# Kernel optimization log

Measured on AMD Instinct MI355X. Metric: run time of the kernel, lower is better.

Reference implementation:

```python
import jax, jax.numpy as jnp
import numpy as np

DIM = 1024
HEADS = 8
NUM_EXPERTS = 65536
NUM_KEYS = 256  # sqrt(NUM_EXPERTS)
DIM_KEY = 512
TOPK = 16  # product_key_topk == num_experts_per_head


def setup_inputs() -> dict:
    key = jax.random.key(0)
    ks = jax.random.split(key, 6)
    B, N = 2, 512
    x = jax.random.normal(ks[0], (B, N, DIM), dtype=jnp.float32)
    gamma = jnp.ones((DIM,), dtype=jnp.float32)
    wq = jax.random.normal(ks[1], (2 * HEADS * DIM_KEY, DIM), dtype=jnp.float32) * 0.02
    keys = jax.random.normal(ks[2], (HEADS, NUM_KEYS, 2, DIM_KEY), dtype=jnp.float32) * 0.02
    table_down = jax.random.normal(ks[3], (NUM_EXPERTS, DIM), dtype=jnp.float32) * 0.02
    table_up = jax.random.normal(ks[4], (NUM_EXPERTS, DIM), dtype=jnp.float32) * 0.02
    return {"x": x, "gamma": gamma, "wq": wq, "keys": keys,
            "table_down": table_down, "table_up": table_up}


def _rmsnorm(v, g):
    # torch F.normalize(x, dim=-1) * gamma * sqrt(dim)
    scale = jnp.sqrt(jnp.asarray(v.shape[-1], v.dtype))
    n = jnp.maximum(jnp.linalg.norm(v, axis=-1, keepdims=True), 1e-12)
    return v / n * g * scale


def reference(x, gamma, wq, keys, table_down, table_up):
    B, N, D = x.shape
    xn = _rmsnorm(x, gamma)          # pre_rmsnorm on x
    gate = xn                        # x_in_gate is None -> gate = norm(x)
    # queries: b n (p h d) -> p b n h d
    q = gate @ wq.T                  # [B,N,2*H*DK]
    q = q.reshape(B, N, 2, HEADS, DIM_KEY).transpose(2, 0, 1, 3, 4)  # [2,B,N,H,DK]
    # sim: p b n h d, h k p d -> p b n h k
    sim = jnp.einsum('pbnhd,hkpd->pbnhk', q, keys)
    sx, ix = jax.lax.top_k(sim[0], TOPK)  # [B,N,H,TOPK]
    sy, iy = jax.lax.top_k(sim[1], TOPK)
    # outer sums over the two product-key axes -> [B,N,H,TOPK*TOPK]
    all_scores = (sx[..., :, None] + sy[..., None, :]).reshape(B, N, HEADS, TOPK * TOPK)
    all_indices = (ix[..., :, None] * NUM_KEYS + iy[..., None, :]).reshape(B, N, HEADS, TOPK * TOPK)
    scores, pk = jax.lax.top_k(all_scores, TOPK)           # [B,N,H,K]
    indices = jnp.take_along_axis(all_indices, pk, axis=-1)  # expert ids [B,N,H,K]
    wd = table_down[indices]  # [B,N,H,K,D]
    wu = table_up[indices]    # [B,N,H,K,D]
    h = jnp.einsum('bnd,bnhkd->bnhk', xn, wd)
    h = jax.nn.gelu(h, approximate=False) * jax.nn.softmax(scores, axis=-1)
    out = jnp.einsum('bnhk,bnhkd->bnd', h, wu)
    return out
```

## Files before the change

kernel.cpp:

```cpp
#include <hip/hip_runtime.h>
#include <math.h>


#define DIMV 1024

__global__ __launch_bounds__(256) void peer_rmsnorm(const float* __restrict__ x,
                                                    const float* __restrict__ gamma,
                                                    float* __restrict__ xnf)
{
    int t = blockIdx.x;
    int tid = threadIdx.x;
    const float4* xr = (const float4*)(x + (size_t)t * DIMV);
    float4 v = xr[tid];
    double ss = (double)v.x*v.x + (double)v.y*v.y + (double)v.z*v.z + (double)v.w*v.w;
    #pragma unroll
    for (int off = 32; off > 0; off >>= 1) ss += __shfl_xor(ss, off);
    __shared__ double red[4];
    if ((tid & 63) == 0) red[tid >> 6] = ss;
    __syncthreads();
    double tot = red[0] + red[1] + red[2] + red[3];
    float n32 = (float)fmax(sqrt(tot), 1e-12);
    const float4* g4 = (const float4*)gamma;
    float4 gv = g4[tid];
    float4 o;
    o.x = __fmul_rn(__fmul_rn(__fdiv_rn(v.x, n32), gv.x), 32.0f);
    o.y = __fmul_rn(__fmul_rn(__fdiv_rn(v.y, n32), gv.y), 32.0f);
    o.z = __fmul_rn(__fmul_rn(__fdiv_rn(v.z, n32), gv.z), 32.0f);
    o.w = __fmul_rn(__fmul_rn(__fdiv_rn(v.w, n32), gv.w), 32.0f);
    ((float4*)(xnf + (size_t)t * DIMV))[tid] = o;
}

__global__ __launch_bounds__(256) void peer_qgemm(const float* __restrict__ A,
                                                  const float* __restrict__ Bm,
                                                  float* __restrict__ C)
{
    __shared__ float As[2][8][80];
    __shared__ float Bs[2][8][160];
    int tid = threadIdx.x;
    int m0 = blockIdx.y * 64, n0 = blockIdx.x * 128;
    int tx = tid & 15, ty = tid >> 4;
    int rb = tid >> 1, hb = (tid & 1) * 4;
    int ra = rb & 63;
    int ca = 5 * (ra >> 2) + (ra & 3);
    int cb = 5 * (rb >> 2) + (rb & 3);
    float acc[4][8] = {};
    float4 av, bv;
    if (tid < 128) av = *(const float4*)(A  + (long)(m0 + ra) * 1024 + hb);
    bv = *(const float4*)(Bm + (long)(n0 + rb) * 1024 + hb);
    if (tid < 128) {
        #pragma unroll
        for (int j = 0; j < 4; j++) As[0][hb + j][ca] = ((const float*)&av)[j];
    }
    #pragma unroll
    for (int j = 0; j < 4; j++) Bs[0][hb + j][cb] = ((const float*)&bv)[j];
    int cur = 0;
    for (int k0 = 0; k0 < 1024; k0 += 8) {
        __syncthreads();
        bool more = (k0 + 8) < 1024;
        if (more) {
            if (tid < 128) av = *(const float4*)(A  + (long)(m0 + ra) * 1024 + (k0 + 8 + hb));
            bv = *(const float4*)(Bm + (long)(n0 + rb) * 1024 + (k0 + 8 + hb));
        }
        #pragma unroll
        for (int kk = 0; kk < 8; kk++) {
            float4 a0 = *(const float4*)&As[cur][kk][5 * ty];
            float4 b0 = *(const float4*)&Bs[cur][kk][10 * tx];
            float4 b1 = *(const float4*)&Bs[cur][kk][10 * tx + 5];
            float ra4[4] = {a0.x, a0.y, a0.z, a0.w};
            float rb8[8] = {b0.x, b0.y, b0.z, b0.w, b1.x, b1.y, b1.z, b1.w};
            #pragma unroll
            for (int i = 0; i < 4; i++)
                #pragma unroll
                for (int j = 0; j < 8; j++)
                    acc[i][j] = __fmaf_rn(ra4[i], rb8[j], acc[i][j]);
        }
        __syncthreads();
        if (more) {
            int nxt = cur ^ 1;
            if (tid < 128) {
                #pragma unroll
                for (int j = 0; j < 4; j++) As[nxt][hb + j][ca] = ((const float*)&av)[j];
            }
            #pragma unroll
            for (int j = 0; j < 4; j++) Bs[nxt][hb + j][cb] = ((const float*)&bv)[j];
            cur = nxt;
        }
    }
    #pragma unroll
    for (int i = 0; i < 4; i++) {
        float4 c0 = {acc[i][0], acc[i][1], acc[i][2], acc[i][3]};
        float4 c1 = {acc[i][4], acc[i][5], acc[i][6], acc[i][7]};
        long r = (long)(m0 + ty * 4 + i) * 8192 + (n0 + tx * 8);
        *(float4*)(C + r)     = c0;
        *(float4*)(C + r + 4) = c1;
    }
}

__global__ __launch_bounds__(256) void peer_sim(const float* __restrict__ qf,
                                                const float* __restrict__ keys,
                                                float* __restrict__ simf)
{
    int tb = blockIdx.x;
    int z  = blockIdx.y;
    int h = z & 7, p = z >> 3;
    int tid = threadIdx.x;
    __shared__ float4 qs[16][128];
    int t0 = tb * 16;
    long qbase = (long)h * 512 + (long)p * 4096;
    int row = tid >> 4, c0 = (tid & 15) * 8;
    const float4* qrow = (const float4*)(qf + (long)(t0 + row) * 8192 + qbase);
    #pragma unroll
    for (int u = 0; u < 8; u++) qs[row][c0 + u] = qrow[c0 + u];
    __syncthreads();
    int k = tid;
    const float4* krow = (const float4*)(keys + (long)h * 262144 + (long)k * 1024 + (long)p * 512);
    float pa[16][4] = {};
    for (int d4 = 0; d4 < 128; d4++) {
        float4 kv = krow[d4];
        #pragma unroll
        for (int tt = 0; tt < 16; tt++) {
            float4 qv = qs[tt][d4];
            pa[tt][0] = __fadd_rn(pa[tt][0], __fmul_rn(qv.x, kv.x));
            pa[tt][1] = __fadd_rn(pa[tt][1], __fmul_rn(qv.y, kv.y));
            pa[tt][2] = __fadd_rn(pa[tt][2], __fmul_rn(qv.z, kv.z));
            pa[tt][3] = __fadd_rn(pa[tt][3], __fmul_rn(qv.w, kv.w));
        }
    }
    #pragma unroll
    for (int tt = 0; tt < 16; tt++) {
        float s = __fadd_rn(__fadd_rn(pa[tt][0], pa[tt][2]),
                            __fadd_rn(pa[tt][1], pa[tt][3]));
        simf[(long)(t0 + tt) * 4096 + (long)p * 2048 + h * 256 + k] = s;
    }
}

__device__ inline void peer_select16(float v[4], int lane, float* outv, int* outi)
{
    for (int iter = 0; iter < 16; iter++) {
        float bv = -INFINITY; int bk = 1 << 30;
        #pragma unroll
        for (int i = 0; i < 4; i++) {
            int k = i * 64 + lane;
            if (v[i] > bv || (v[i] == bv && k < bk)) { bv = v[i]; bk = k; }
        }
        #pragma unroll
        for (int off = 32; off > 0; off >>= 1) {
            float ov = __shfl_xor(bv, off);
            int   ok = __shfl_xor(bk, off);
            if (ov > bv || (ov == bv && ok < bk)) { bv = ov; bk = ok; }
        }
        if (lane == 0) { outv[iter] = bv; outi[iter] = bk; }
        __syncthreads();
        if ((bk & 63) == lane) v[bk >> 6] = -INFINITY;
    }
}

__global__ __launch_bounds__(64) void peer_topk(const float* __restrict__ sim,
                                                float* __restrict__ wsel,
                                                int* __restrict__ esel)
{
    int b = blockIdx.x;
    int t = b >> 3, h = b & 7;
    int lane = threadIdx.x;
    const float* simx = sim + (size_t)t * 4096 + h * 256;
    const float* simy = simx + 2048;
    __shared__ float sxv[16]; __shared__ int sxi[16];
    __shared__ float syv[16]; __shared__ int syi[16];
    __shared__ float cv[16];  __shared__ int cf[16];
    float v[4];
    #pragma unroll
    for (int i = 0; i < 4; i++) v[i] = simx[i*64 + lane];
    peer_select16(v, lane, sxv, sxi);
    __syncthreads();
    #pragma unroll
    for (int i = 0; i < 4; i++) v[i] = simy[i*64 + lane];
    peer_select16(v, lane, syv, syi);
    __syncthreads();
    #pragma unroll
    for (int i = 0; i < 4; i++) {
        int f = i*64 + lane;
        v[i] = __fadd_rn(sxv[f >> 4], syv[f & 15]);
    }
    peer_select16(v, lane, cv, cf);
    __syncthreads();
    double m = (double)cv[0];
    double w = (lane < 16) ? exp((double)cv[lane] - m) : 0.0;
    double Z = w;
    #pragma unroll
    for (int off = 32; off > 0; off >>= 1) Z += __shfl_xor(Z, off);
    if (lane < 16) {
        int f = cf[lane];
        esel[b * 16 + lane] = sxi[f >> 4] * 256 + syi[f & 15];
        wsel[b * 16 + lane] = (float)(w / Z);
    }
}

__global__ __launch_bounds__(256) void peer_down(const float* __restrict__ xn,
                                                 const float* __restrict__ table_down,
                                                 const int* __restrict__ esel,
                                                 const float* __restrict__ wsel,
                                                 float* __restrict__ g)
{
    int tid = threadIdx.x;
    int wv = (blockIdx.x << 2) | (tid >> 6);
    int lane = tid & 63;
    int t = wv >> 7;
    __shared__ float4 xs[256];
    xs[tid] = ((const float4*)(xn + (size_t)t * DIMV))[tid];
    __syncthreads();
    int e = esel[wv];
    const float4* dr = (const float4*)(table_down + (size_t)e * DIMV);
    double acc = 0.0;
    #pragma unroll
    for (int it = 0; it < 4; it++) {
        int d4 = it * 64 + lane;
        float4 a = xs[d4];
        float4 bb = dr[d4];
        acc = fma((double)a.x, (double)bb.x, acc);
        acc = fma((double)a.y, (double)bb.y, acc);
        acc = fma((double)a.z, (double)bb.z, acc);
        acc = fma((double)a.w, (double)bb.w, acc);
    }
    #pragma unroll
    for (int off = 32; off > 0; off >>= 1) acc += __shfl_xor(acc, off);
    if (lane == 0) {
        double hv = acc;
        double ge = 0.5 * hv * (1.0 + erf(hv * 0.70710678118654752));
        g[wv] = (float)(ge * (double)wsel[wv]);
    }
}

__global__ __launch_bounds__(64) void peer_up(const float* __restrict__ table_up,
                                              const int* __restrict__ esel,
                                              const float* __restrict__ gbuf,
                                              float* __restrict__ out)
{
    int t  = blockIdx.x >> 2;
    int ds = blockIdx.x & 3;
    int lane = threadIdx.x;
    __shared__ float gs[128];
    __shared__ int   es[128];
    gs[lane]      = gbuf[t * 128 + lane];
    gs[lane + 64] = gbuf[t * 128 + 64 + lane];
    es[lane]      = esel[t * 128 + lane];
    es[lane + 64] = esel[t * 128 + 64 + lane];
    __syncthreads();
    int dbase = ds * 256 + lane * 4;
    double a0 = 0, a1 = 0, a2 = 0, a3 = 0;
    for (int j = 0; j < 128; j++) {
        const float4 u = *(const float4*)(table_up + (size_t)es[j] * DIMV + dbase);
        double gj = (double)gs[j];
        a0 = fma(gj, (double)u.x, a0); a1 = fma(gj, (double)u.y, a1);
        a2 = fma(gj, (double)u.z, a2); a3 = fma(gj, (double)u.w, a3);
    }
    float4 o = {(float)a0, (float)a1, (float)a2, (float)a3};
    *(float4*)(out + (size_t)t * DIMV + dbase) = o;
}

extern "C" void kernel_launch(void* const* d_in, const int* in_sizes, int n_in,
                              void* d_out, int out_size, void* d_ws, size_t ws_size,
                              hipStream_t stream)
{
    const float* x          = (const float*)d_in[0];
    const float* gamma      = (const float*)d_in[1];
    const float* wq         = (const float*)d_in[2];
    const float* keys       = (const float*)d_in[3];
    const float* table_down = (const float*)d_in[4];
    const float* table_up   = (const float*)d_in[5];
    float* out = (float*)d_out;
    char* wsb  = (char*)d_ws;

    float* xnf  = (float*)(wsb);
    float* qf   = (float*)(wsb + (4ull<<20));
    float* simf = (float*)(wsb + (36ull<<20));
    float* wsel = (float*)(wsb + (52ull<<20));
    int*   esel = (int*)  (wsb + (52ull<<20) + (512ull<<10));
    float* g    = (float*)(wsb + (53ull<<20));
    if (ws_size < (54ull << 20)) return;

    peer_rmsnorm<<<1024, 256, 0, stream>>>(x, gamma, xnf);

    peer_qgemm<<<dim3(64, 16, 1), 256, 0, stream>>>(xnf, wq, qf);

    peer_sim<<<dim3(64, 16, 1), 256, 0, stream>>>(qf, keys, simf);

    peer_topk<<<8192, 64, 0, stream>>>(simf, wsel, esel);

    peer_down<<<32768, 256, 0, stream>>>(xnf, table_down, esel, wsel, g);

    peer_up<<<4096, 64, 0, stream>>>(table_up, esel, g, out);
}
```

Baseline: 608.9 us.

## Enlarge query GEMM tile to 128x128 with 8x8 register blocking

Changes the query-projection GEMM from 64x128 to 128x128 output tiles, with each thread computing an 8x8 block instead of 4x8. The shared-memory layout drops its padded indexing, and all threads now load both A and B. One of the two barriers per K-step is removed. The aim is to raise arithmetic intensity per shared-memory and global load, at the cost of more registers, half as many blocks, and possible bank conflicts on the transposed shared-memory stores.

```diff
diff --git a/kernel.cpp b/kernel.cpp
--- a/kernel.cpp
+++ b/kernel.cpp
@@ -34,65 +34,60 @@
                                                   const float* __restrict__ Bm,
                                                   float* __restrict__ C)
 {
-    __shared__ float As[2][8][80];
-    __shared__ float Bs[2][8][160];
-    int tid = threadIdx.x;
-    int m0 = blockIdx.y * 64, n0 = blockIdx.x * 128;
+    __shared__ float As[2][8][128];
+    __shared__ float Bs[2][8][128];
+    int tid = threadIdx.x;
+    int m0 = blockIdx.y * 128, n0 = blockIdx.x * 128;
     int tx = tid & 15, ty = tid >> 4;
-    int rb = tid >> 1, hb = (tid & 1) * 4;
-    int ra = rb & 63;
-    int ca = 5 * (ra >> 2) + (ra & 3);
-    int cb = 5 * (rb >> 2) + (rb & 3);
-    float acc[4][8] = {};
-    float4 av, bv;
-    if (tid < 128) av = *(const float4*)(A  + (long)(m0 + ra) * 1024 + hb);
-    bv = *(const float4*)(Bm + (long)(n0 + rb) * 1024 + hb);
-    if (tid < 128) {
-        #pragma unroll
-        for (int j = 0; j < 4; j++) As[0][hb + j][ca] = ((const float*)&av)[j];
-    }
-    #pragma unroll
-    for (int j = 0; j < 4; j++) Bs[0][hb + j][cb] = ((const float*)&bv)[j];
+    int lrow = tid >> 1, lk = (tid & 1) * 4;
+    float acc[8][8] = {};
+    float4 av = *(const float4*)(A  + (long)(m0 + lrow) * 1024 + lk);
+    float4 bv = *(const float4*)(Bm + (long)(n0 + lrow) * 1024 + lk);
+    #pragma unroll
+    for (int j = 0; j < 4; j++) {
+        As[0][lk + j][lrow] = ((const float*)&av)[j];
+        Bs[0][lk + j][lrow] = ((const float*)&bv)[j];
+    }
+    __syncthreads();
     int cur = 0;
     for (int k0 = 0; k0 < 1024; k0 += 8) {
-        __syncthreads();
         bool more = (k0 + 8) < 1024;
         if (more) {
-            if (tid < 128) av = *(const float4*)(A  + (long)(m0 + ra) * 1024 + (k0 + 8 + hb));
-            bv = *(const float4*)(Bm + (long)(n0 + rb) * 1024 + (k0 + 8 + hb));
+            av = *(const float4*)(A  + (long)(m0 + lrow) * 1024 + (k0 + 8 + lk));
+            bv = *(const float4*)(Bm + (long)(n0 + lrow) * 1024 + (k0 + 8 + lk));
         }
         #pragma unroll
         for (int kk = 0; kk < 8; kk++) {
-            float4 a0 = *(const float4*)&As[cur][kk][5 * ty];
-            float4 b0 = *(const float4*)&Bs[cur][kk][10 * tx];
-            float4 b1 = *(const float4*)&Bs[cur][kk][10 * tx + 5];
-            float ra4[4] = {a0.x, a0.y, a0.z, a0.w};
-            float rb8[8] = {b0.x, b0.y, b0.z, b0.w, b1.x, b1.y, b1.z, b1.w};
+            float4 a0 = *(const float4*)&As[cur][kk][ty * 8];
+            float4 a1 = *(const float4*)&As[cur][kk][ty * 8 + 4];
+            float4 b0 = *(const float4*)&Bs[cur][kk][tx * 4];
+            float4 b1 = *(const float4*)&Bs[cur][kk][tx * 4 + 64];
+            float ra8[8] = {a0.x,a0.y,a0.z,a0.w,a1.x,a1.y,a1.z,a1.w};
+            float rb8[8] = {b0.x,b0.y,b0.z,b0.w,b1.x,b1.y,b1.z,b1.w};
             #pragma unroll
-            for (int i = 0; i < 4; i++)
+            for (int i = 0; i < 8; i++)
                 #pragma unroll
                 for (int j = 0; j < 8; j++)
-                    acc[i][j] = __fmaf_rn(ra4[i], rb8[j], acc[i][j]);
-        }
-        __syncthreads();
+                    acc[i][j] = __fmaf_rn(ra8[i], rb8[j], acc[i][j]);
+        }
         if (more) {
             int nxt = cur ^ 1;
-            if (tid < 128) {
-                #pragma unroll
-                for (int j = 0; j < 4; j++) As[nxt][hb + j][ca] = ((const float*)&av)[j];
+            #pragma unroll
+            for (int j = 0; j < 4; j++) {
+                As[nxt][lk + j][lrow] = ((const float*)&av)[j];
+                Bs[nxt][lk + j][lrow] = ((const float*)&bv)[j];
             }
-            #pragma unroll
-            for (int j = 0; j < 4; j++) Bs[nxt][hb + j][cb] = ((const float*)&bv)[j];
+            __syncthreads();
             cur = nxt;
         }
     }
     #pragma unroll
-    for (int i = 0; i < 4; i++) {
+    for (int i = 0; i < 8; i++) {
         float4 c0 = {acc[i][0], acc[i][1], acc[i][2], acc[i][3]};
         float4 c1 = {acc[i][4], acc[i][5], acc[i][6], acc[i][7]};
-        long r = (long)(m0 + ty * 4 + i) * 8192 + (n0 + tx * 8);
-        *(float4*)(C + r)     = c0;
-        *(float4*)(C + r + 4) = c1;
+        long r = (long)(m0 + ty * 8 + i) * 8192 + n0;
+        *(float4*)(C + r + tx * 4)      = c0;
+        *(float4*)(C + r + 64 + tx * 4) = c1;
     }
 }
 
@@ -280,7 +275,7 @@
 
     peer_rmsnorm<<<1024, 256, 0, stream>>>(x, gamma, xnf);
 
-    peer_qgemm<<<dim3(64, 16, 1), 256, 0, stream>>>(xnf, wq, qf);
+    peer_qgemm<<<dim3(64, 8, 1), 256, 0, stream>>>(xnf, wq, qf);
 
     peer_sim<<<dim3(64, 16, 1), 256, 0, stream>>>(qf, keys, simf);
 
```

Result: faster. 557.3 us (-8.5%).
